# Kernel tuning notes

Hardware: AMD Instinct MI355X
Metric: run time of the kernel (lower is better)

## Reference

```python
import jax, jax.numpy as jnp
import numpy as np

EMB_DIM = 128
WEIGHT_COL = 24

def setup_inputs() -> dict:
    key = jax.random.key(0)
    ks = jax.random.split(key, 9)
    B, S = 8, 4096
    s_in = 1.0 / np.sqrt(EMB_DIM)
    s_out = 1.0 / np.sqrt(WEIGHT_COL)
    return {
        "x": jax.random.normal(ks[0], (B, S, EMB_DIM), dtype=jnp.float32),
        "wQ": jax.random.uniform(ks[1], (EMB_DIM, WEIGHT_COL), jnp.float32, -s_in, s_in),
        "bQ": jax.random.uniform(ks[2], (WEIGHT_COL,), jnp.float32, -s_in, s_in),
        "wK": jax.random.uniform(ks[3], (EMB_DIM, WEIGHT_COL), jnp.float32, -s_in, s_in),
        "bK": jax.random.uniform(ks[4], (WEIGHT_COL,), jnp.float32, -s_in, s_in),
        "wV": jax.random.uniform(ks[5], (EMB_DIM, WEIGHT_COL), jnp.float32, -s_in, s_in),
        "bV": jax.random.uniform(ks[6], (WEIGHT_COL,), jnp.float32, -s_in, s_in),
        "wO": jax.random.uniform(ks[7], (WEIGHT_COL, EMB_DIM), jnp.float32, -s_out, s_out),
        "bO": jax.random.uniform(ks[8], (EMB_DIM,), jnp.float32, -s_out, s_out),
    }

def reference(x, wQ, bQ, wK, bK, wV, bV, wO, bO):
    # projections: [B,S,E] -> [B,S,D]
    Q = x @ wQ + bQ
    K = x @ wK + bK
    V = x @ wV + bV
    # NOTE: source scales by sqrt(emb_dim), not sqrt(weight_col)
    scale = 1.0 / np.sqrt(EMB_DIM).astype(np.float32)
    scores = jnp.einsum('bqd,bkd->bqk', Q, K) * scale  # [B,S,S]
    A = jax.nn.softmax(scores, axis=-1)
    H = jnp.einsum('bqk,bkd->bqd', A, V)               # [B,S,D]
    return H @ wO + bO                                  # [B,S,E]
```

## Files before the change

kernel.cpp:

```cpp
#include <hip/hip_runtime.h>


#define B_ 8
#define S_ 4096
#define E_ 128
#define D_ 24
#define N_ (B_ * S_)
#define SCALE 0.08838834764831845f
#define LOG2E 1.4426950408889634f

#define TK 64
#define KS_STRIDE 40
#define VS_STRIDE 136
#define HS_STRIDE 40
#define XS_STRIDE 136
#define OS_STRIDE 84

typedef __attribute__((ext_vector_type(8))) short bfrag;
typedef __attribute__((ext_vector_type(4))) float ffrag;

__device__ inline unsigned short f2bf(float f) {
    unsigned int x = __builtin_bit_cast(unsigned int, f);
    return (unsigned short)((x + 0x7fffu + ((x >> 16) & 1u)) >> 16);
}
__device__ inline unsigned int pack2(float a, float b) {
    return (unsigned int)f2bf(a) | ((unsigned int)f2bf(b) << 16);
}
__device__ inline unsigned int pack2h(float a, float b) {
    unsigned int ua = __builtin_bit_cast(unsigned int, a) + 0x8000u;
    unsigned int ub = __builtin_bit_cast(unsigned int, b) + 0x8000u;
    return __builtin_amdgcn_perm(ub, ua, 0x07060302);
}

__global__ __launch_bounds__(256) void prep_kernel(
    const float* __restrict__ wQ, const float* __restrict__ bQ,
    const float* __restrict__ wK, const float* __restrict__ bK,
    const float* __restrict__ wV, const float* __restrict__ bV,
    const float* __restrict__ wO,
    unsigned short* __restrict__ Wf, unsigned short* __restrict__ wOf,
    float* __restrict__ bqkv)
{
    const int gtid   = blockIdx.x * 256 + threadIdx.x;
    const int stride = gridDim.x * 256;
    const float qs = SCALE * LOG2E;
    for (int idx = gtid; idx < 4 * 5 * 512; idx += stride) {
        const int j    = idx & 7;
        const int lane = (idx >> 3) & 63;
        const int nt   = (idx >> 9) % 5;
        const int kt   = idx / 2560;
        const int n = nt * 16 + (lane & 15);
        const int k = kt * 32 + ((lane >> 4) << 3) + j;
        float v = 0.0f;
        if (n < 24)      v = wQ[k * 24 + n] * qs;
        else if (n < 48) v = wK[k * 24 + (n - 24)];
        else if (n < 72) v = wV[k * 24 + (n - 48)];
        Wf[idx] = f2bf(v);
    }
    for (int idx = gtid; idx < 8 * 512; idx += stride) {
        const int j    = idx & 7;
        const int lane = (idx >> 3) & 63;
        const int nt   = idx >> 9;
        const int k = ((lane >> 4) << 3) + j;
        const int e = nt * 16 + (lane & 15);
        wOf[idx] = (k < 24) ? f2bf(wO[k * 128 + e]) : (unsigned short)0;
    }
    if (gtid < 80) {
        float v = 0.0f;
        if (gtid < 24)      v = bQ[gtid] * qs;
        else if (gtid < 48) v = bK[gtid - 24];
        else if (gtid < 72) v = bV[gtid - 48];
        bqkv[gtid] = v;
    }
}

__global__ __launch_bounds__(256) void proj_kernel(
    const float* __restrict__ x, const unsigned short* __restrict__ Wf,
    const float* __restrict__ bqkv,
    unsigned short* __restrict__ Qbf, unsigned short* __restrict__ Kbf,
    unsigned short* __restrict__ Vt)
{
    __shared__ float smem[64 * OS_STRIDE];
    unsigned short* xs = (unsigned short*)smem;
    float* os = smem;

    const int tid  = threadIdx.x;
    const int lane = tid & 63;
    const int w    = tid >> 6;
    const int col  = lane & 15;
    const int quad = lane >> 4;
    const int rb   = blockIdx.x * 64;

    #pragma unroll
    for (int i = 0; i < 8; ++i) {
        const int idx = i * 256 + tid;
        const int row = idx >> 5, c4 = idx & 31;
        const float4 xv = *(const float4*)(x + (size_t)(rb + row) * 128 + c4 * 4);
        uint2 h;
        h.x = pack2(xv.x, xv.y);
        h.y = pack2(xv.z, xv.w);
        *(uint2*)(&xs[row * XS_STRIDE + c4 * 4]) = h;
    }

    bfrag Wfr[20];
    #pragma unroll
    for (int f = 0; f < 20; ++f)
        Wfr[f] = *(const bfrag*)(Wf + (f * 64 + lane) * 8);

    __syncthreads();

    ffrag acc[5];
    #pragma unroll
    for (int nt = 0; nt < 5; ++nt) acc[nt] = (ffrag){0.f, 0.f, 0.f, 0.f};

    #pragma unroll
    for (int kt = 0; kt < 4; ++kt) {
        const bfrag Af = *(const bfrag*)(&xs[(w * 16 + col) * XS_STRIDE + kt * 32 + quad * 8]);
        #pragma unroll
        for (int nt = 0; nt < 5; ++nt)
            acc[nt] = __builtin_amdgcn_mfma_f32_16x16x32_bf16(Af, Wfr[kt * 5 + nt], acc[nt], 0, 0, 0);
    }

    __syncthreads();

    #pragma unroll
    for (int nt = 0; nt < 5; ++nt) {
        const float bb = bqkv[nt * 16 + col];
        #pragma unroll
        for (int r = 0; r < 4; ++r)
            os[(w * 16 + quad * 4 + r) * OS_STRIDE + nt * 16 + col] = acc[nt][r] + bb;
    }
    __syncthreads();

    {
        const int half  = tid & 1;
        const int row   = (tid >> 1) & 63;
        const int isK   = tid >> 7;
        const int cbase = isK * 24;
        unsigned int pk[8];
        #pragma unroll
        for (int g = 0; g < 8; ++g) {
            const int c0 = half * 16 + g * 2;
            const float f0 = (c0     < 24) ? os[row * OS_STRIDE + cbase + c0]     : 0.0f;
            const float f1 = (c0 + 1 < 24) ? os[row * OS_STRIDE + cbase + c0 + 1] : 0.0f;
            pk[g] = pack2(f0, f1);
        }
        unsigned short* dst = (isK ? Kbf : Qbf) + (size_t)(rb + row) * 32 + half * 16;
        *(uint4*)(dst)     = make_uint4(pk[0], pk[1], pk[2], pk[3]);
        *(uint4*)(dst + 8) = make_uint4(pk[4], pk[5], pk[6], pk[7]);
    }

    if (tid < 192) {
        const int d  = tid % 24;
        const int ch = tid / 24;
        unsigned int p[4];
        #pragma unroll
        for (int g = 0; g < 4; ++g) {
            const float f0 = os[(ch * 8 + g * 2 + 0) * OS_STRIDE + 48 + d];
            const float f1 = os[(ch * 8 + g * 2 + 1) * OS_STRIDE + 48 + d];
            p[g] = pack2(f0, f1);
        }
        const int b = rb >> 12, s0 = rb & 4095;
        uint4* dst = (uint4*)(Vt + (((size_t)(b * 24 + d)) << 12) + s0 + ch * 8);
        *dst = make_uint4(p[0], p[1], p[2], p[3]);
    }
}

__global__ __launch_bounds__(256, 8) void attn_kernel(
    const unsigned short* __restrict__ Qbf, const unsigned short* __restrict__ Kbf,
    const unsigned short* __restrict__ Vt,
    float* __restrict__ Opart, float* __restrict__ lpart)
{
    __shared__ unsigned short Ks[TK * KS_STRIDE];
    __shared__ unsigned short Vs[32 * VS_STRIDE];

    const int tid    = threadIdx.x;
    const int lane   = tid & 63;
    const int w      = tid >> 6;
    const int col    = lane & 15;
    const int quad   = lane >> 4;
    const int blk    = blockIdx.x;
    const int split  = blockIdx.y;
    const int nsp    = gridDim.y;
    const int kchunk = S_ / nsp;
    const int b      = blk >> 6;
    const int qbase  = blk * 64 + w * 16;

    #pragma unroll
    for (int i0 = 0; i0 < 3; ++i0) {
        const int i = i0 * 256 + tid;
        if (i < 32 * VS_STRIDE / 8)
            *(uint4*)(&Vs[i * 8]) = make_uint4(0u, 0u, 0u, 0u);
    }

    const bfrag Qf = *(const bfrag*)(Qbf + (size_t)(qbase + col) * 32 + quad * 8);

    ffrag Ot0 = {0.f, 0.f, 0.f, 0.f};
    ffrag Ot1 = {0.f, 0.f, 0.f, 0.f};
    float lacc = 0.0f;

    const unsigned short* Kbase = Kbf + ((size_t)(b * 4096) + split * kchunk) * 32;
    const unsigned short* Vbase = Vt + (size_t)(b * 24) * 4096 + split * kchunk;

    __syncthreads();

    for (int kb = 0; kb < kchunk; kb += TK) {
        {
            const int key = tid >> 2, ch = tid & 3;
            const uint4 t4 = *(const uint4*)(Kbase + (size_t)(kb + key) * 32 + ch * 8);
            *(uint4*)(&Ks[key * KS_STRIDE + ch * 8]) = t4;
        }
        #pragma unroll
        for (int u0 = 0; u0 < 2; ++u0) {
            const int u = u0 * 256 + tid;
            if (u < 384) {
                const int d = u >> 4, cq = u & 15, c = cq >> 2, qd = cq & 3;
                const uint2 t2 = *(const uint2*)(Vbase + (size_t)d * 4096 + kb + c * 16 + qd * 4);
                *(uint2*)(&Vs[d * VS_STRIDE + c * 32 + qd * 8]) = t2;
            }
        }
        __syncthreads();

        #pragma unroll
        for (int c = 0; c < 4; ++c) {
            const bfrag Kf = *(const bfrag*)(&Ks[(c * 16 + col) * KS_STRIDE + quad * 8]);
            ffrag S = {0.f, 0.f, 0.f, 0.f};
            S = __builtin_amdgcn_mfma_f32_16x16x32_bf16(Kf, Qf, S, 0, 0, 0);
            const float p0 = __builtin_amdgcn_exp2f(S[0]);
            const float p1 = __builtin_amdgcn_exp2f(S[1]);
            const float p2 = __builtin_amdgcn_exp2f(S[2]);
            const float p3 = __builtin_amdgcn_exp2f(S[3]);
            lacc += (p0 + p1) + (p2 + p3);
            union { bfrag f; unsigned int u[4]; } P;
            P.u[0] = pack2h(p0, p1);
            P.u[1] = pack2h(p2, p3);
            P.u[2] = 0u; P.u[3] = 0u;
            const bfrag Va0 = *(const bfrag*)(&Vs[col * VS_STRIDE + c * 32 + quad * 8]);
            const bfrag Va1 = *(const bfrag*)(&Vs[(16 + col) * VS_STRIDE + c * 32 + quad * 8]);
            Ot0 = __builtin_amdgcn_mfma_f32_16x16x32_bf16(Va0, P.f, Ot0, 0, 0, 0);
            Ot1 = __builtin_amdgcn_mfma_f32_16x16x32_bf16(Va1, P.f, Ot1, 0, 0, 0);
        }
        __syncthreads();
    }

    float v = lacc;
    v += __shfl_xor(v, 16);
    v += __shfl_xor(v, 32);
    if (quad == 0)
        lpart[(size_t)split * N_ + qbase + col] = v;

    const size_t base = ((size_t)split * N_ + qbase + col) * 32;
    *(ffrag*)(&Opart[base + quad * 4]) = Ot0;
    if (quad < 2)
        *(ffrag*)(&Opart[base + 16 + quad * 4]) = Ot1;
}

__global__ __launch_bounds__(256) void combine_kernel(
    const float* __restrict__ Opart, const float* __restrict__ lpart,
    const unsigned short* __restrict__ wOf, const float* __restrict__ bO,
    float* __restrict__ out, int nsp)
{
    __shared__ unsigned short Hs[64 * HS_STRIDE];

    const int tid = threadIdx.x;
    const int qb  = blockIdx.x * 64;
    {
        const int ql = tid >> 2;
        const int c8 = (tid & 3) * 8;
        const int q  = qb + ql;
        float a[8] = {0.f, 0.f, 0.f, 0.f, 0.f, 0.f, 0.f, 0.f};
        if (c8 < 24) {
            for (int s = 0; s < nsp; ++s) {
                const float* p = &Opart[((size_t)s * N_ + q) * 32 + c8];
                const float4 u = *(const float4*)p;
                const float4 v = *(const float4*)(p + 4);
                a[0] += u.x; a[1] += u.y; a[2] += u.z; a[3] += u.w;
                a[4] += v.x; a[5] += v.y; a[6] += v.z; a[7] += v.w;
            }
        }
        float ls = 0.f;
        for (int s = 0; s < nsp; ++s) ls += lpart[(size_t)s * N_ + q];
        const float inv = 1.0f / ls;
        uint4 pk;
        pk.x = pack2(a[0] * inv, a[1] * inv);
        pk.y = pack2(a[2] * inv, a[3] * inv);
        pk.z = pack2(a[4] * inv, a[5] * inv);
        pk.w = pack2(a[6] * inv, a[7] * inv);
        *(uint4*)(&Hs[ql * HS_STRIDE + c8]) = pk;
    }
    __syncthreads();

    const int lane = tid & 63;
    const int w    = tid >> 6;
    const int col  = lane & 15;
    const int quad = lane >> 4;
    const bfrag Hf = *(const bfrag*)(&Hs[(w * 16 + col) * HS_STRIDE + quad * 8]);
    #pragma unroll
    for (int nt = 0; nt < 8; ++nt) {
        const bfrag Wo = *(const bfrag*)(wOf + (nt * 64 + lane) * 8);
        ffrag C = {0.f, 0.f, 0.f, 0.f};
        C = __builtin_amdgcn_mfma_f32_16x16x32_bf16(Hf, Wo, C, 0, 0, 0);
        const float bo = bO[nt * 16 + col];
        #pragma unroll
        for (int r = 0; r < 4; ++r)
            out[(size_t)(qb + w * 16 + quad * 4 + r) * 128 + nt * 16 + col] = C[r] + bo;
    }
}

extern "C" void kernel_launch(void* const* d_in, const int* in_sizes, int n_in,
                              void* d_out, int out_size, void* d_ws, size_t ws_size,
                              hipStream_t stream) {
    const float* x  = (const float*)d_in[0];
    const float* wQ = (const float*)d_in[1];
    const float* bQ = (const float*)d_in[2];
    const float* wK = (const float*)d_in[3];
    const float* bK = (const float*)d_in[4];
    const float* wV = (const float*)d_in[5];
    const float* bV = (const float*)d_in[6];
    const float* wO = (const float*)d_in[7];
    const float* bO = (const float*)d_in[8];
    float* out = (float*)d_out;

    unsigned short* ws16 = (unsigned short*)d_ws;
    unsigned short* Qbf = ws16;
    unsigned short* Kbf = Qbf + (size_t)N_ * 32;
    unsigned short* Vt  = Kbf + (size_t)N_ * 32;
    unsigned short* Wf  = Vt + (size_t)B_ * 24 * S_;
    unsigned short* wOf = Wf + 4 * 5 * 512;
    float* bqkv = (float*)(wOf + 8 * 512);
    float* Opart = bqkv + 80;
    const size_t baseBytes = (size_t)((char*)Opart - (char*)d_ws);

    int nsp = 4;
    while (nsp > 1) {
        const size_t need = baseBytes + (size_t)nsp * N_ * 32 * 4 + (size_t)nsp * N_ * 4;
        if (need <= ws_size) break;
        nsp >>= 1;
    }
    float* lpart = Opart + (size_t)nsp * N_ * 32;

    prep_kernel<<<8, 256, 0, stream>>>(wQ, bQ, wK, bK, wV, bV, wO, Wf, wOf, bqkv);
    proj_kernel<<<N_ / 64, 256, 0, stream>>>(x, Wf, bqkv, Qbf, Kbf, Vt);
    attn_kernel<<<dim3(N_ / 64, nsp), 256, 0, stream>>>(Qbf, Kbf, Vt, Opart, lpart);
    combine_kernel<<<N_ / 64, 256, 0, stream>>>(Opart, lpart, wOf, bO, out, nsp);
}
```

Before: 136.0 us.

## Fill full MFMA K-dim with two score tiles and compute row sums via ones-row

```diff
diff --git a/kernel.cpp b/kernel.cpp
--- a/kernel.cpp
+++ b/kernel.cpp
@@ -9,7 +9,7 @@
 #define SCALE 0.08838834764831845f
 #define LOG2E 1.4426950408889634f
 
-#define TK 64
+#define TK 128
 #define KS_STRIDE 40
 #define VS_STRIDE 136
 #define HS_STRIDE 40
@@ -185,18 +185,14 @@
     const int b      = blk >> 6;
     const int qbase  = blk * 64 + w * 16;
 
-    #pragma unroll
-    for (int i0 = 0; i0 < 3; ++i0) {
-        const int i = i0 * 256 + tid;
-        if (i < 32 * VS_STRIDE / 8)
-            *(uint4*)(&Vs[i * 8]) = make_uint4(0u, 0u, 0u, 0u);
-    }
+    if (tid < 16)
+        *(uint4*)(&Vs[24 * VS_STRIDE + tid * 8]) =
+            make_uint4(0x3F803F80u, 0x3F803F80u, 0x3F803F80u, 0x3F803F80u);
 
     const bfrag Qf = *(const bfrag*)(Qbf + (size_t)(qbase + col) * 32 + quad * 8);
 
     ffrag Ot0 = {0.f, 0.f, 0.f, 0.f};
     ffrag Ot1 = {0.f, 0.f, 0.f, 0.f};
-    float lacc = 0.0f;
 
     const unsigned short* Kbase = Kbf + ((size_t)(b * 4096) + split * kchunk) * 32;
     const unsigned short* Vbase = Vt + (size_t)(b * 24) * 4096 + split * kchunk;
@@ -204,54 +200,61 @@
     __syncthreads();
 
     for (int kb = 0; kb < kchunk; kb += TK) {
-        {
-            const int key = tid >> 2, ch = tid & 3;
+        #pragma unroll
+        for (int i = 0; i < 2; ++i) {
+            const int idx = i * 256 + tid;
+            const int key = idx >> 2, ch = idx & 3;
             const uint4 t4 = *(const uint4*)(Kbase + (size_t)(kb + key) * 32 + ch * 8);
-            *(uint4*)(&Ks[key * KS_STRIDE + ch * 8]) = t4;
-        }
-        #pragma unroll
-        for (int u0 = 0; u0 < 2; ++u0) {
-            const int u = u0 * 256 + tid;
+            const int row = (key & ~31) + (((key >> 2) & 1) << 4)
+                          + (((key & 31) >> 3) << 2) + (key & 3);
+            *(uint4*)(&Ks[row * KS_STRIDE + ch * 8]) = t4;
+        }
+        #pragma unroll
+        for (int i = 0; i < 2; ++i) {
+            const int u = i * 256 + tid;
             if (u < 384) {
-                const int d = u >> 4, cq = u & 15, c = cq >> 2, qd = cq & 3;
-                const uint2 t2 = *(const uint2*)(Vbase + (size_t)d * 4096 + kb + c * 16 + qd * 4);
-                *(uint2*)(&Vs[d * VS_STRIDE + c * 32 + qd * 8]) = t2;
+                const int d = u >> 4, ch = u & 15;
+                const uint4 t4 = *(const uint4*)(Vbase + (size_t)d * 4096 + kb + ch * 8);
+                *(uint4*)(&Vs[d * VS_STRIDE + ch * 8]) = t4;
             }
         }
         __syncthreads();
 
         #pragma unroll
-        for (int c = 0; c < 4; ++c) {
-            const bfrag Kf = *(const bfrag*)(&Ks[(c * 16 + col) * KS_STRIDE + quad * 8]);
-            ffrag S = {0.f, 0.f, 0.f, 0.f};
-            S = __builtin_amdgcn_mfma_f32_16x16x32_bf16(Kf, Qf, S, 0, 0, 0);
-            const float p0 = __builtin_amdgcn_exp2f(S[0]);
-            const float p1 = __builtin_amdgcn_exp2f(S[1]);
-            const float p2 = __builtin_amdgcn_exp2f(S[2]);
-            const float p3 = __builtin_amdgcn_exp2f(S[3]);
-            lacc += (p0 + p1) + (p2 + p3);
+        for (int c2 = 0; c2 < 4; ++c2) {
+            const bfrag Kfe = *(const bfrag*)(&Ks[(c2 * 32 + col) * KS_STRIDE + quad * 8]);
+            const bfrag Kfo = *(const bfrag*)(&Ks[(c2 * 32 + 16 + col) * KS_STRIDE + quad * 8]);
+            ffrag Se = {0.f, 0.f, 0.f, 0.f};
+            ffrag So = {0.f, 0.f, 0.f, 0.f};
+            Se = __builtin_amdgcn_mfma_f32_16x16x32_bf16(Kfe, Qf, Se, 0, 0, 0);
+            So = __builtin_amdgcn_mfma_f32_16x16x32_bf16(Kfo, Qf, So, 0, 0, 0);
+            const float pe0 = __builtin_amdgcn_exp2f(Se[0]);
+            const float pe1 = __builtin_amdgcn_exp2f(Se[1]);
+            const float pe2 = __builtin_amdgcn_exp2f(Se[2]);
+            const float pe3 = __builtin_amdgcn_exp2f(Se[3]);
+            const float po0 = __builtin_amdgcn_exp2f(So[0]);
+            const float po1 = __builtin_amdgcn_exp2f(So[1]);
+            const float po2 = __builtin_amdgcn_exp2f(So[2]);
+            const float po3 = __builtin_amdgcn_exp2f(So[3]);
             union { bfrag f; unsigned int u[4]; } P;
-            P.u[0] = pack2h(p0, p1);
-            P.u[1] = pack2h(p2, p3);
-            P.u[2] = 0u; P.u[3] = 0u;
-            const bfrag Va0 = *(const bfrag*)(&Vs[col * VS_STRIDE + c * 32 + quad * 8]);
-            const bfrag Va1 = *(const bfrag*)(&Vs[(16 + col) * VS_STRIDE + c * 32 + quad * 8]);
+            P.u[0] = pack2h(pe0, pe1);
+            P.u[1] = pack2h(pe2, pe3);
+            P.u[2] = pack2h(po0, po1);
+            P.u[3] = pack2h(po2, po3);
+            const bfrag Va0 = *(const bfrag*)(&Vs[col * VS_STRIDE + c2 * 32 + quad * 8]);
+            const bfrag Va1 = *(const bfrag*)(&Vs[(16 + col) * VS_STRIDE + c2 * 32 + quad * 8]);
             Ot0 = __builtin_amdgcn_mfma_f32_16x16x32_bf16(Va0, P.f, Ot0, 0, 0, 0);
             Ot1 = __builtin_amdgcn_mfma_f32_16x16x32_bf16(Va1, P.f, Ot1, 0, 0, 0);
         }
         __syncthreads();
     }
-
-    float v = lacc;
-    v += __shfl_xor(v, 16);
-    v += __shfl_xor(v, 32);
-    if (quad == 0)
-        lpart[(size_t)split * N_ + qbase + col] = v;
 
     const size_t base = ((size_t)split * N_ + qbase + col) * 32;
     *(ffrag*)(&Opart[base + quad * 4]) = Ot0;
     if (quad < 2)
         *(ffrag*)(&Opart[base + 16 + quad * 4]) = Ot1;
+    if (quad == 2)
+        lpart[(size_t)split * N_ + qbase + col] = Ot1[0];
 }
 
 __global__ __launch_bounds__(256) void combine_kernel(
```

Measured after the change: 125.1 us. 1.09x faster.
